# Kernel tuning notes

Measured on AMD Instinct MI355X. Metric: run time of the kernel, lower is better.

Reference implementation:

```python
import jax, jax.numpy as jnp
import numpy as np

E, T, D_IN, D_HID, D_OUT = 8, 2048, 1024, 4096, 1024
INTER = 2 * D_HID  # gated (SwiGLU) -> weight1 produces [gate, val]


def setup_inputs() -> dict:
    key = jax.random.key(0)
    k_x, k_w1, k_w2 = jax.random.split(key, 3)
    # kaiming_uniform-ish scale for weights
    x = jax.random.normal(k_x, (E, T, D_IN), dtype=jnp.float32)
    w1 = jax.random.normal(k_w1, (E, D_IN, INTER), dtype=jnp.float32) * (1.0 / np.sqrt(D_IN))
    w2 = jax.random.normal(k_w2, (E, D_HID, D_OUT), dtype=jnp.float32) * (1.0 / np.sqrt(D_HID))
    return {"x": x, "weight1": w1, "weight2": w2}


def reference(x, weight1, weight2):
    # h: [E, T, 2*D_HID] grouped GEMM over experts
    h = jnp.einsum("etd,edi->eti", x, weight1)
    gate, val = jnp.split(h, 2, axis=-1)
    h = jax.nn.silu(gate) * val  # SwiGLU; dropout is identity in eval / p=0
    out = jnp.einsum("eth,eho->eto", h, weight2)  # [E, T, D_OUT]
    return out
```

## Files before the change

### kernel.cpp

```cpp
#include <hip/hip_runtime.h>


#define E_    8
#define T_    2048
#define DIN   1024
#define DHID  4096
#define DOUT  1024
#define INTER 8192

typedef _Float16 f16;
typedef _Float16 f16x8 __attribute__((ext_vector_type(8)));
typedef float    f32x4 __attribute__((ext_vector_type(4)));

typedef const __attribute__((address_space(1))) void gvoid_t;
typedef __attribute__((address_space(3))) void lvoid_t;

__device__ __forceinline__ void gload_lds16(const void* g, void* l) {
  __builtin_amdgcn_global_load_lds((gvoid_t*)g, (lvoid_t*)l, 16, 0, 0);
}

__global__ __launch_bounds__(256) void conv_f32_f16(
    const float* __restrict__ src, f16* __restrict__ dst, int n8) {
  int i = blockIdx.x * 256 + threadIdx.x;
  int stride = gridDim.x * 256;
  for (; i < n8; i += stride) {
    const float4* s = (const float4*)(src + (size_t)i * 8);
    float4 a0 = s[0], a1 = s[1];
    f16x8 v;
    v[0] = (f16)a0.x; v[1] = (f16)a0.y; v[2] = (f16)a0.z; v[3] = (f16)a0.w;
    v[4] = (f16)a1.x; v[5] = (f16)a1.y; v[6] = (f16)a1.z; v[7] = (f16)a1.w;
    *(f16x8*)(dst + (size_t)i * 8) = v;
  }
}

__global__ __launch_bounds__(256) void xpose_f32_f16(
    const float* __restrict__ src, f16* __restrict__ dst,
    int R, int C, int tR, int tC) {
  __shared__ f16 tile[32][33];
  int bid = blockIdx.x;
  int perE = tR * tC;
  int e = bid / perE;
  int rem = bid - e * perE;
  int rt = rem / tC;
  int ct = rem - rt * tC;
  int r0 = rt * 32, c0 = ct * 32;
  int t = threadIdx.x;
  int lr = t >> 5, lc = t & 31;
  const float* s = src + (size_t)e * R * C;
  f16* d = dst + (size_t)e * C * R;
#pragma unroll
  for (int i = 0; i < 4; ++i) {
    int r = lr + 8 * i;
    tile[r][lc] = (f16)s[(size_t)(r0 + r) * C + (c0 + lc)];
  }
  __syncthreads();
#pragma unroll
  for (int i = 0; i < 4; ++i) {
    int r = lr + 8 * i;
    d[(size_t)(c0 + r) * R + (r0 + lc)] = tile[lc][r];
  }
}

__global__ __launch_bounds__(512, 2) void gemm1_swiglu_xh(
    const f16* __restrict__ xh,
    const f16* __restrict__ w1t,
    f16* __restrict__ hact) {
  __shared__ f16 As[128][32];
  __shared__ f16 Bg[128][32];
  __shared__ f16 Bv[128][32];

  int bid = blockIdx.x;
  int e   = bid >> 9;
  int rem = bid & 511;
  int mt  = rem >> 5;
  int nt  = rem & 31;
  int m0 = mt * 128, n0 = nt * 128;

  const f16* xe = xh  + ((size_t)e * T_ + m0) * DIN;
  const f16* wg = w1t + ((size_t)e * INTER + n0) * DIN;
  const f16* wv = w1t + ((size_t)e * INTER + DHID + n0) * DIN;

  int tid  = threadIdx.x;
  int lane = tid & 63;
  int wid  = tid >> 6;

  int srow = wid * 16 + (lane >> 2);
  int scol = (lane & 3) * 8;
  f16* lA = &As[wid * 16][0];
  f16* lG = &Bg[wid * 16][0];
  f16* lV = &Bv[wid * 16][0];

  int wm = wid >> 2;
  int wn = wid & 3;
  int lr = lane & 15;
  int lk = (lane >> 4) * 8;

  f32x4 accG[4][2], accV[4][2];
#pragma unroll
  for (int m = 0; m < 4; ++m)
#pragma unroll
    for (int n = 0; n < 2; ++n) {
      accG[m][n] = f32x4{0.f, 0.f, 0.f, 0.f};
      accV[m][n] = f32x4{0.f, 0.f, 0.f, 0.f};
    }

  for (int k = 0; k < DIN; k += 32) {
    __syncthreads();
    gload_lds16(xe + (size_t)srow * DIN + k + scol, lA);
    gload_lds16(wg + (size_t)srow * DIN + k + scol, lG);
    gload_lds16(wv + (size_t)srow * DIN + k + scol, lV);
    __syncthreads();

    f16x8 af[4], bg[2], bv[2];
#pragma unroll
    for (int m = 0; m < 4; ++m)
      af[m] = *(const f16x8*)&As[wm * 64 + m * 16 + lr][lk];
#pragma unroll
    for (int n = 0; n < 2; ++n) {
      bg[n] = *(const f16x8*)&Bg[wn * 32 + n * 16 + lr][lk];
      bv[n] = *(const f16x8*)&Bv[wn * 32 + n * 16 + lr][lk];
    }
#pragma unroll
    for (int m = 0; m < 4; ++m)
#pragma unroll
      for (int n = 0; n < 2; ++n) {
        accG[m][n] = __builtin_amdgcn_mfma_f32_16x16x32_f16(af[m], bg[n], accG[m][n], 0, 0, 0);
        accV[m][n] = __builtin_amdgcn_mfma_f32_16x16x32_f16(af[m], bv[n], accV[m][n], 0, 0, 0);
      }
  }

  f16* he = hact + (size_t)e * T_ * DHID;
  int rbase = m0 + wm * 64 + (lane >> 4) * 4;
  int cbase = n0 + wn * 32 + lr;
#pragma unroll
  for (int m = 0; m < 4; ++m)
#pragma unroll
    for (int n = 0; n < 2; ++n)
#pragma unroll
      for (int j = 0; j < 4; ++j) {
        int row = rbase + m * 16 + j;
        int col = cbase + n * 16;
        float g = accG[m][n][j];
        float v = accV[m][n][j];
        float s = g / (1.0f + __expf(-g));
        he[(size_t)row * DHID + col] = (f16)(s * v);
      }
}

__global__ __launch_bounds__(512, 2) void gemm1_swiglu_rs(
    const float* __restrict__ x,
    const f16* __restrict__ w1t,
    f16* __restrict__ hact) {
  __shared__ f16 As[128][36];
  __shared__ f16 Bg[128][32];
  __shared__ f16 Bv[128][32];

  int bid = blockIdx.x;
  int e   = bid >> 9;
  int rem = bid & 511;
  int mt  = rem >> 5;
  int nt  = rem & 31;
  int m0 = mt * 128, n0 = nt * 128;

  const float* xe = x   + ((size_t)e * T_ + m0) * DIN;
  const f16*   wg = w1t + ((size_t)e * INTER + n0) * DIN;
  const f16*   wv = w1t + ((size_t)e * INTER + DHID + n0) * DIN;

  int tid  = threadIdx.x;
  int lane = tid & 63;
  int wid  = tid >> 6;

  int arow = tid >> 2;
  int acol = (tid & 3) * 8;
  int brow = wid * 16 + (lane >> 2);
  int bcol = (lane & 3) * 8;
  f16* lG = &Bg[wid * 16][0];
  f16* lV = &Bv[wid * 16][0];

  int wm = wid >> 2;
  int wn = wid & 3;
  int lr = lane & 15;
  int lk = (lane >> 4) * 8;

  f32x4 accG[4][2], accV[4][2];
#pragma unroll
  for (int m = 0; m < 4; ++m)
#pragma unroll
    for (int n = 0; n < 2; ++n) {
      accG[m][n] = f32x4{0.f, 0.f, 0.f, 0.f};
      accV[m][n] = f32x4{0.f, 0.f, 0.f, 0.f};
    }

  for (int k = 0; k < DIN; k += 32) {
    __syncthreads();
    gload_lds16(wg + (size_t)brow * DIN + k + bcol, lG);
    gload_lds16(wv + (size_t)brow * DIN + k + bcol, lV);
    {
      const float* sa = xe + (size_t)arow * DIN + k + acol;
      float4 a0 = ((const float4*)sa)[0];
      float4 a1 = ((const float4*)sa)[1];
      f16x8 v;
      v[0] = (f16)a0.x; v[1] = (f16)a0.y; v[2] = (f16)a0.z; v[3] = (f16)a0.w;
      v[4] = (f16)a1.x; v[5] = (f16)a1.y; v[6] = (f16)a1.z; v[7] = (f16)a1.w;
      *(f16x8*)&As[arow][acol] = v;
    }
    __syncthreads();

    f16x8 af[4], bg[2], bv[2];
#pragma unroll
    for (int m = 0; m < 4; ++m)
      af[m] = *(const f16x8*)&As[wm * 64 + m * 16 + lr][lk];
#pragma unroll
    for (int n = 0; n < 2; ++n) {
      bg[n] = *(const f16x8*)&Bg[wn * 32 + n * 16 + lr][lk];
      bv[n] = *(const f16x8*)&Bv[wn * 32 + n * 16 + lr][lk];
    }
#pragma unroll
    for (int m = 0; m < 4; ++m)
#pragma unroll
      for (int n = 0; n < 2; ++n) {
        accG[m][n] = __builtin_amdgcn_mfma_f32_16x16x32_f16(af[m], bg[n], accG[m][n], 0, 0, 0);
        accV[m][n] = __builtin_amdgcn_mfma_f32_16x16x32_f16(af[m], bv[n], accV[m][n], 0, 0, 0);
      }
  }

  f16* he = hact + (size_t)e * T_ * DHID;
  int rbase = m0 + wm * 64 + (lane >> 4) * 4;
  int cbase = n0 + wn * 32 + lr;
#pragma unroll
  for (int m = 0; m < 4; ++m)
#pragma unroll
    for (int n = 0; n < 2; ++n)
#pragma unroll
      for (int j = 0; j < 4; ++j) {
        int row = rbase + m * 16 + j;
        int col = cbase + n * 16;
        float g = accG[m][n][j];
        float v = accV[m][n][j];
        float s = g / (1.0f + __expf(-g));
        he[(size_t)row * DHID + col] = (f16)(s * v);
      }
}

__global__ __launch_bounds__(256) void gemm2(
    const f16* __restrict__ hact,
    const f16* __restrict__ w2t,
    float* __restrict__ out) {
  __shared__ f16 As[128][32];
  __shared__ f16 Bs[128][32];

  int bid = blockIdx.x;
  int e   = bid >> 7;
  int rem = bid & 127;
  int mt  = rem >> 3;
  int nt  = rem & 7;
  int m0 = mt * 128, n0 = nt * 128;

  const f16* ha = hact + ((size_t)e * T_ + m0) * DHID;
  const f16* wb = w2t  + ((size_t)e * DOUT + n0) * DHID;

  int tid  = threadIdx.x;
  int lane = tid & 63;
  int wid  = tid >> 6;

  int srow0 = wid * 32 + (lane >> 2);
  int srow1 = srow0 + 16;
  int scol  = (lane & 3) * 8;
  f16* lA0 = &As[wid * 32][0];
  f16* lA1 = &As[wid * 32 + 16][0];
  f16* lB0 = &Bs[wid * 32][0];
  f16* lB1 = &Bs[wid * 32 + 16][0];

  int wm = wid >> 1;
  int wn = wid & 1;
  int lr = lane & 15;
  int lk = (lane >> 4) * 8;

  f32x4 acc[4][4];
#pragma unroll
  for (int m = 0; m < 4; ++m)
#pragma unroll
    for (int n = 0; n < 4; ++n) acc[m][n] = f32x4{0.f, 0.f, 0.f, 0.f};

  for (int k = 0; k < DHID; k += 32) {
    __syncthreads();
    gload_lds16(ha + (size_t)srow0 * DHID + k + scol, lA0);
    gload_lds16(ha + (size_t)srow1 * DHID + k + scol, lA1);
    gload_lds16(wb + (size_t)srow0 * DHID + k + scol, lB0);
    gload_lds16(wb + (size_t)srow1 * DHID + k + scol, lB1);
    __syncthreads();

    f16x8 af[4], bf[4];
#pragma unroll
    for (int m = 0; m < 4; ++m)
      af[m] = *(const f16x8*)&As[wm * 64 + m * 16 + lr][lk];
#pragma unroll
    for (int n = 0; n < 4; ++n)
      bf[n] = *(const f16x8*)&Bs[wn * 64 + n * 16 + lr][lk];
#pragma unroll
    for (int m = 0; m < 4; ++m)
#pragma unroll
      for (int n = 0; n < 4; ++n)
        acc[m][n] = __builtin_amdgcn_mfma_f32_16x16x32_f16(af[m], bf[n], acc[m][n], 0, 0, 0);
  }

  float* oe = out + (size_t)e * T_ * DOUT;
  int rbase = m0 + wm * 64 + (lane >> 4) * 4;
  int cbase = n0 + wn * 64 + lr;
#pragma unroll
  for (int m = 0; m < 4; ++m)
#pragma unroll
    for (int n = 0; n < 4; ++n)
#pragma unroll
      for (int j = 0; j < 4; ++j) {
        int row = rbase + m * 16 + j;
        int col = cbase + n * 16;
        oe[(size_t)row * DOUT + col] = acc[m][n][j];
      }
}

extern "C" void kernel_launch(void* const* d_in, const int* in_sizes, int n_in,
                              void* d_out, int out_size, void* d_ws, size_t ws_size,
                              hipStream_t stream) {
  const float* x  = (const float*)d_in[0];
  const float* w1 = (const float*)d_in[1];
  const float* w2 = (const float*)d_in[2];
  float* out = (float*)d_out;

  const size_t HACT_B = (size_t)E_ * T_ * DHID * 2;
  const size_t WT_B   = (size_t)E_ * INTER * DIN * 2;
  const size_t XH_B   = (size_t)E_ * T_ * DIN * 2;

  f16* hact = (f16*)d_ws;
  f16* wt   = (f16*)((char*)d_ws + HACT_B);

  xpose_f32_f16<<<E_ * (DIN / 32) * (INTER / 32), 256, 0, stream>>>(
      w1, wt, DIN, INTER, DIN / 32, INTER / 32);

  if (ws_size >= HACT_B + WT_B + XH_B) {
    f16* xxh = (f16*)((char*)d_ws + HACT_B + WT_B);
    conv_f32_f16<<<2048, 256, 0, stream>>>(x, xxh, E_ * T_ * DIN / 8);
    gemm1_swiglu_xh<<<E_ * 16 * 32, 512, 0, stream>>>(xxh, wt, hact);
  } else {
    gemm1_swiglu_rs<<<E_ * 16 * 32, 512, 0, stream>>>(x, wt, hact);
  }

  xpose_f32_f16<<<E_ * (DHID / 32) * (DOUT / 32), 256, 0, stream>>>(
      w2, wt, DHID, DOUT, DHID / 32, DOUT / 32);
  gemm2<<<E_ * 16 * 8, 256, 0, stream>>>(hact, wt, out);
}
```

Measured before the change: 685.5 us.

## Rewrite gemm1 SwiGLU kernel as 256x128 double-buffered eight-phase pipeline

Replaces the single-buffered 128x128, K=32 gemm1 kernel with a 256x128 tile using K=64 steps. LDS is double-buffered and XOR-swizzled, and global-to-LDS loads are interleaved across eight phases with MFMA bursts under raised wave priority. Block IDs are also remapped so consecutive blocks spread across experts. The aim is to hide global load latency, cut LDS bank conflicts and halve the number of A/B loads per output. In exchange it uses more registers (128 accumulators) and LDS, and relies on fragile hand-written vmcnt and barrier scheduling.

After: 682.2 us. About the same (-0.5%).

```diff
diff --git a/kernel.cpp b/kernel.cpp
--- a/kernel.cpp
+++ b/kernel.cpp
@@ -61,20 +61,21 @@
   }
 }
 
-__global__ __launch_bounds__(512, 2) void gemm1_swiglu_xh(
+__global__ __launch_bounds__(512, 2) void gemm1_swiglu_8ph(
     const f16* __restrict__ xh,
     const f16* __restrict__ w1t,
     f16* __restrict__ hact) {
-  __shared__ f16 As[128][32];
-  __shared__ f16 Bg[128][32];
-  __shared__ f16 Bv[128][32];
-
-  int bid = blockIdx.x;
-  int e   = bid >> 9;
-  int rem = bid & 511;
+  __shared__ __align__(1024) f16 As [2][256][64];
+  __shared__ __align__(1024) f16 Bgs[2][128][64];
+  __shared__ __align__(1024) f16 Bvs[2][128][64];
+
+  int bid0 = blockIdx.x;
+  int bid  = (bid0 & 7) * 256 + (bid0 >> 3);
+  int e   = bid >> 8;
+  int rem = bid & 255;
   int mt  = rem >> 5;
   int nt  = rem & 31;
-  int m0 = mt * 128, n0 = nt * 128;
+  int m0 = mt * 256, n0 = nt * 128;
 
   const f16* xe = xh  + ((size_t)e * T_ + m0) * DIN;
   const f16* wg = w1t + ((size_t)e * INTER + n0) * DIN;
@@ -83,57 +84,144 @@
   int tid  = threadIdx.x;
   int lane = tid & 63;
   int wid  = tid >> 6;
-
-  int srow = wid * 16 + (lane >> 2);
-  int scol = (lane & 3) * 8;
-  f16* lA = &As[wid * 16][0];
-  f16* lG = &Bg[wid * 16][0];
-  f16* lV = &Bv[wid * 16][0];
-
-  int wm = wid >> 2;
-  int wn = wid & 3;
-  int lr = lane & 15;
-  int lk = (lane >> 4) * 8;
-
-  f32x4 accG[4][2], accV[4][2];
-#pragma unroll
-  for (int m = 0; m < 4; ++m)
+  int wm   = wid >> 2;
+  int wn   = wid & 3;
+  int lr   = lane & 15;
+  int l16  = lane >> 4;
+
+  int srow = lane >> 3;
+  int scol = ((lane & 7) ^ srow) * 8;
+
+  auto stageA = [&](int buf, int kt, int i) {
+    int ci = wid + 8 * i;
+    gload_lds16(xe + (size_t)(ci * 8 + srow) * DIN + kt * 64 + scol,
+                (char*)&As[buf][0][0] + ci * 1024);
+  };
+  auto stageG = [&](int buf, int kt, int i) {
+    int ci = wid + 8 * i;
+    gload_lds16(wg + (size_t)(ci * 8 + srow) * DIN + kt * 64 + scol,
+                (char*)&Bgs[buf][0][0] + ci * 1024);
+  };
+  auto stageV = [&](int buf, int kt, int i) {
+    int ci = wid + 8 * i;
+    gload_lds16(wv + (size_t)(ci * 8 + srow) * DIN + kt * 64 + scol,
+                (char*)&Bvs[buf][0][0] + ci * 1024);
+  };
+
+  f32x4 accG[8][2], accV[8][2];
+#pragma unroll
+  for (int m = 0; m < 8; ++m)
 #pragma unroll
     for (int n = 0; n < 2; ++n) {
       accG[m][n] = f32x4{0.f, 0.f, 0.f, 0.f};
       accV[m][n] = f32x4{0.f, 0.f, 0.f, 0.f};
     }
 
-  for (int k = 0; k < DIN; k += 32) {
-    __syncthreads();
-    gload_lds16(xe + (size_t)srow * DIN + k + scol, lA);
-    gload_lds16(wg + (size_t)srow * DIN + k + scol, lG);
-    gload_lds16(wv + (size_t)srow * DIN + k + scol, lV);
-    __syncthreads();
-
-    f16x8 af[4], bg[2], bv[2];
-#pragma unroll
-    for (int m = 0; m < 4; ++m)
-      af[m] = *(const f16x8*)&As[wm * 64 + m * 16 + lr][lk];
-#pragma unroll
-    for (int n = 0; n < 2; ++n) {
-      bg[n] = *(const f16x8*)&Bg[wn * 32 + n * 16 + lr][lk];
-      bv[n] = *(const f16x8*)&Bv[wn * 32 + n * 16 + lr][lk];
-    }
-#pragma unroll
-    for (int m = 0; m < 4; ++m)
-#pragma unroll
-      for (int n = 0; n < 2; ++n) {
-        accG[m][n] = __builtin_amdgcn_mfma_f32_16x16x32_f16(af[m], bg[n], accG[m][n], 0, 0, 0);
-        accV[m][n] = __builtin_amdgcn_mfma_f32_16x16x32_f16(af[m], bv[n], accV[m][n], 0, 0, 0);
-      }
-  }
+  f16x8 af[4][2], bg[2][2], bv[2][2];
+
+#define READ_AF(b, MH)                                                       \
+  _Pragma("unroll") for (int m = 0; m < 4; ++m)                              \
+  _Pragma("unroll") for (int kk = 0; kk < 2; ++kk) {                         \
+    int row_ = wm * 128 + (MH) * 64 + m * 16 + lr;                           \
+    af[m][kk] = *(const f16x8*)((const char*)&As[b][0][0] + row_ * 128 +     \
+                                (((kk * 4 + l16) ^ (lr & 7)) << 4));         \
+  }
+#define READ_B(ARR, DST, b)                                                  \
+  _Pragma("unroll") for (int n = 0; n < 2; ++n)                              \
+  _Pragma("unroll") for (int kk = 0; kk < 2; ++kk) {                         \
+    int row_ = wn * 32 + n * 16 + lr;                                        \
+    DST[n][kk] = *(const f16x8*)((const char*)&ARR[b][0][0] + row_ * 128 +   \
+                                 (((kk * 4 + l16) ^ (lr & 7)) << 4));        \
+  }
+#define MFMA16(ACC, BB, MH)                                                  \
+  __builtin_amdgcn_s_setprio(1);                                            \
+  _Pragma("unroll") for (int m = 0; m < 4; ++m)                              \
+  _Pragma("unroll") for (int n = 0; n < 2; ++n)                              \
+  _Pragma("unroll") for (int kk = 0; kk < 2; ++kk)                          \
+    ACC[(MH) * 4 + m][n] = __builtin_amdgcn_mfma_f32_16x16x32_f16(           \
+        af[m][kk], BB[n][kk], ACC[(MH) * 4 + m][n], 0, 0, 0);                \
+  __builtin_amdgcn_s_setprio(0);
+#define BAR() __builtin_amdgcn_s_barrier()
+#define LGKM0() asm volatile("s_waitcnt lgkmcnt(0)" ::: "memory")
+#define VM6() asm volatile("s_waitcnt vmcnt(6)" ::: "memory")
+
+  stageA(0, 0, 0); stageA(0, 0, 1); stageA(0, 0, 2); stageA(0, 0, 3);
+  stageG(0, 0, 0); stageG(0, 0, 1);
+  stageV(0, 0, 0); stageV(0, 0, 1);
+  stageA(1, 1, 0); stageA(1, 1, 1);
+  stageG(1, 1, 0); stageG(1, 1, 1);
+  stageV(1, 1, 0); stageV(1, 1, 1);
+  VM6();
+  BAR();
+
+  for (int it = 0; it < 8; ++it) {
+    int tb = 2 * it + 1;
+    int pa = (2 * it + 2) & 15;
+    int pb = (2 * it + 3) & 15;
+
+    READ_AF(0, 0);
+    READ_B(Bgs, bg, 0);
+    stageA(1, tb, 2); stageA(1, tb, 3);
+    BAR(); LGKM0();
+    MFMA16(accG, bg, 0);
+    BAR();
+
+    READ_B(Bvs, bv, 0);
+    stageG(0, pa, 0); stageG(0, pa, 1);
+    BAR(); LGKM0();
+    MFMA16(accV, bv, 0);
+    BAR();
+
+    READ_AF(0, 1);
+    stageV(0, pa, 0); stageV(0, pa, 1);
+    BAR(); LGKM0();
+    MFMA16(accG, bg, 1);
+    BAR();
+
+    stageA(0, pa, 0); stageA(0, pa, 1);
+    BAR();
+    MFMA16(accV, bv, 1);
+    VM6();
+    BAR();
+
+    READ_AF(1, 0);
+    READ_B(Bgs, bg, 1);
+    stageA(0, pa, 2); stageA(0, pa, 3);
+    BAR(); LGKM0();
+    MFMA16(accG, bg, 0);
+    BAR();
+
+    READ_B(Bvs, bv, 1);
+    stageG(1, pb, 0); stageG(1, pb, 1);
+    BAR(); LGKM0();
+    MFMA16(accV, bv, 0);
+    BAR();
+
+    READ_AF(1, 1);
+    stageV(1, pb, 0); stageV(1, pb, 1);
+    BAR(); LGKM0();
+    MFMA16(accG, bg, 1);
+    BAR();
+
+    stageA(1, pb, 0); stageA(1, pb, 1);
+    BAR();
+    MFMA16(accV, bv, 1);
+    VM6();
+    BAR();
+  }
+
+#undef READ_AF
+#undef READ_B
+#undef MFMA16
+#undef BAR
+#undef LGKM0
+#undef VM6
 
   f16* he = hact + (size_t)e * T_ * DHID;
-  int rbase = m0 + wm * 64 + (lane >> 4) * 4;
+  int rbase = m0 + wm * 128 + l16 * 4;
   int cbase = n0 + wn * 32 + lr;
 #pragma unroll
-  for (int m = 0; m < 4; ++m)
+  for (int m = 0; m < 8; ++m)
 #pragma unroll
     for (int n = 0; n < 2; ++n)
 #pragma unroll
@@ -340,7 +428,7 @@
   if (ws_size >= HACT_B + WT_B + XH_B) {
     f16* xxh = (f16*)((char*)d_ws + HACT_B + WT_B);
     conv_f32_f16<<<2048, 256, 0, stream>>>(x, xxh, E_ * T_ * DIN / 8);
-    gemm1_swiglu_xh<<<E_ * 16 * 32, 512, 0, stream>>>(xxh, wt, hact);
+    gemm1_swiglu_8ph<<<E_ * 8 * 32, 512, 0, stream>>>(xxh, wt, hact);
   } else {
     gemm1_swiglu_rs<<<E_ * 16 * 32, 512, 0, stream>>>(x, wt, hact);
   }
```

## Rewrite gemm2 as 256x256 double-buffered 8-phase pipelined MFMA kernel

Applied to the files above, without the earlier changes.

Replaces the simple single-buffered 128x128 GEMM2 with a 256x256-tile, 512-thread kernel. It uses K=64 double-buffered LDS tiles with XOR swizzling and issues global-to-LDS loads interleaved across eight barrier-separated phases. MFMA priority is raised during the math phases. The aim is to overlap memory traffic with compute, raise reuse per loaded byte, and avoid LDS bank conflicts, at the cost of higher register and LDS use and fewer blocks.

Result: faster. 600.4 us (-12.4%).

```diff
diff --git a/kernel.cpp b/kernel.cpp
--- a/kernel.cpp
+++ b/kernel.cpp
@@ -242,19 +242,19 @@
       }
 }
 
-__global__ __launch_bounds__(256) void gemm2(
+__global__ __launch_bounds__(512, 2) void gemm2_8ph(
     const f16* __restrict__ hact,
     const f16* __restrict__ w2t,
     float* __restrict__ out) {
-  __shared__ f16 As[128][32];
-  __shared__ f16 Bs[128][32];
+  __shared__ __align__(1024) f16 As[2][256][64];
+  __shared__ __align__(1024) f16 Bs[2][256][64];
 
   int bid = blockIdx.x;
-  int e   = bid >> 7;
-  int rem = bid & 127;
-  int mt  = rem >> 3;
-  int nt  = rem & 7;
-  int m0 = mt * 128, n0 = nt * 128;
+  int e   = bid >> 5;
+  int rem = bid & 31;
+  int mt  = rem >> 2;
+  int nt  = rem & 3;
+  int m0 = mt * 256, n0 = nt * 256;
 
   const f16* ha = hact + ((size_t)e * T_ + m0) * DHID;
   const f16* wb = w2t  + ((size_t)e * DOUT + n0) * DHID;
@@ -262,53 +262,132 @@
   int tid  = threadIdx.x;
   int lane = tid & 63;
   int wid  = tid >> 6;
-
-  int srow0 = wid * 32 + (lane >> 2);
-  int srow1 = srow0 + 16;
-  int scol  = (lane & 3) * 8;
-  f16* lA0 = &As[wid * 32][0];
-  f16* lA1 = &As[wid * 32 + 16][0];
-  f16* lB0 = &Bs[wid * 32][0];
-  f16* lB1 = &Bs[wid * 32 + 16][0];
-
-  int wm = wid >> 1;
-  int wn = wid & 1;
-  int lr = lane & 15;
-  int lk = (lane >> 4) * 8;
-
-  f32x4 acc[4][4];
-#pragma unroll
-  for (int m = 0; m < 4; ++m)
+  int wm   = wid >> 2;
+  int wn   = wid & 3;
+  int lr   = lane & 15;
+  int l16  = lane >> 4;
+
+  int srow = lane >> 3;
+  int scol = ((lane & 7) ^ srow) * 8;
+
+  auto stA = [&](int buf, int kt, int i) {
+    int ci = wid + 8 * i;
+    gload_lds16(ha + (size_t)(ci * 8 + srow) * DHID + kt * 64 + scol,
+                (char*)&As[buf][0][0] + ci * 1024);
+  };
+  auto stB = [&](int buf, int kt, int i) {
+    int ci = wid + 8 * i;
+    gload_lds16(wb + (size_t)(ci * 8 + srow) * DHID + kt * 64 + scol,
+                (char*)&Bs[buf][0][0] + ci * 1024);
+  };
+
+  f32x4 acc[8][4];
+#pragma unroll
+  for (int m = 0; m < 8; ++m)
 #pragma unroll
     for (int n = 0; n < 4; ++n) acc[m][n] = f32x4{0.f, 0.f, 0.f, 0.f};
 
-  for (int k = 0; k < DHID; k += 32) {
-    __syncthreads();
-    gload_lds16(ha + (size_t)srow0 * DHID + k + scol, lA0);
-    gload_lds16(ha + (size_t)srow1 * DHID + k + scol, lA1);
-    gload_lds16(wb + (size_t)srow0 * DHID + k + scol, lB0);
-    gload_lds16(wb + (size_t)srow1 * DHID + k + scol, lB1);
-    __syncthreads();
-
-    f16x8 af[4], bf[4];
-#pragma unroll
-    for (int m = 0; m < 4; ++m)
-      af[m] = *(const f16x8*)&As[wm * 64 + m * 16 + lr][lk];
-#pragma unroll
-    for (int n = 0; n < 4; ++n)
-      bf[n] = *(const f16x8*)&Bs[wn * 64 + n * 16 + lr][lk];
-#pragma unroll
-    for (int m = 0; m < 4; ++m)
-#pragma unroll
-      for (int n = 0; n < 4; ++n)
-        acc[m][n] = __builtin_amdgcn_mfma_f32_16x16x32_f16(af[m], bf[n], acc[m][n], 0, 0, 0);
-  }
+  f16x8 af[4][2], bf0[2][2], bf1[2][2];
+
+#define READ_A2(b, MH)                                                       \
+  _Pragma("unroll") for (int m = 0; m < 4; ++m)                              \
+  _Pragma("unroll") for (int kk = 0; kk < 2; ++kk) {                         \
+    int row_ = wm * 128 + (MH) * 64 + m * 16 + lr;                           \
+    af[m][kk] = *(const f16x8*)((const char*)&As[b][0][0] + row_ * 128 +     \
+                                (((kk * 4 + l16) ^ (lr & 7)) << 4));         \
+  }
+#define READ_B2(b, NH, DST)                                                  \
+  _Pragma("unroll") for (int n = 0; n < 2; ++n)                              \
+  _Pragma("unroll") for (int kk = 0; kk < 2; ++kk) {                         \
+    int row_ = wn * 64 + (NH) * 32 + n * 16 + lr;                            \
+    DST[n][kk] = *(const f16x8*)((const char*)&Bs[b][0][0] + row_ * 128 +    \
+                                 (((kk * 4 + l16) ^ (lr & 7)) << 4));        \
+  }
+#define MFMA16Q(MH, NH, BB)                                                  \
+  __builtin_amdgcn_s_setprio(1);                                            \
+  _Pragma("unroll") for (int m = 0; m < 4; ++m)                              \
+  _Pragma("unroll") for (int n = 0; n < 2; ++n)                              \
+  _Pragma("unroll") for (int kk = 0; kk < 2; ++kk)                          \
+    acc[(MH) * 4 + m][(NH) * 2 + n] = __builtin_amdgcn_mfma_f32_16x16x32_f16(\
+        af[m][kk], BB[n][kk], acc[(MH) * 4 + m][(NH) * 2 + n], 0, 0, 0);     \
+  __builtin_amdgcn_s_setprio(0);
+#define BAR() __builtin_amdgcn_s_barrier()
+#define LGKM0() asm volatile("s_waitcnt lgkmcnt(0)" ::: "memory")
+#define VM6() asm volatile("s_waitcnt vmcnt(6)" ::: "memory")
+
+  stA(0, 0, 0); stA(0, 0, 1); stA(0, 0, 2); stA(0, 0, 3);
+  stB(0, 0, 0); stB(0, 0, 1); stB(0, 0, 2); stB(0, 0, 3);
+  stB(1, 1, 0); stB(1, 1, 1); stB(1, 1, 2); stB(1, 1, 3);
+  stA(1, 1, 0); stA(1, 1, 1);
+  VM6();
+  BAR();
+
+  for (int it = 0; it < 32; ++it) {
+    int tb = 2 * it + 1;
+    int pa = (2 * it + 2) & 63;
+    int pb = (2 * it + 3) & 63;
+
+    READ_A2(0, 0); READ_B2(0, 0, bf0);
+    stA(1, tb, 2); stA(1, tb, 3);
+    BAR(); LGKM0();
+    MFMA16Q(0, 0, bf0);
+    BAR();
+
+    READ_B2(0, 1, bf1);
+    BAR(); LGKM0();
+    MFMA16Q(0, 1, bf1);
+    BAR();
+
+    READ_A2(0, 1);
+    stB(0, pa, 0); stB(0, pa, 1);
+    BAR(); LGKM0();
+    MFMA16Q(1, 0, bf0);
+    BAR();
+
+    stB(0, pa, 2); stB(0, pa, 3);
+    stA(0, pa, 0); stA(0, pa, 1);
+    BAR();
+    MFMA16Q(1, 1, bf1);
+    VM6();
+    BAR();
+
+    READ_A2(1, 0); READ_B2(1, 0, bf0);
+    stA(0, pa, 2); stA(0, pa, 3);
+    BAR(); LGKM0();
+    MFMA16Q(0, 0, bf0);
+    BAR();
+
+    READ_B2(1, 1, bf1);
+    BAR(); LGKM0();
+    MFMA16Q(0, 1, bf1);
+    BAR();
+
+    READ_A2(1, 1);
+    stB(1, pb, 0); stB(1, pb, 1);
+    BAR(); LGKM0();
+    MFMA16Q(1, 0, bf0);
+    BAR();
+
+    stB(1, pb, 2); stB(1, pb, 3);
+    stA(1, pb, 0); stA(1, pb, 1);
+    BAR();
+    MFMA16Q(1, 1, bf1);
+    VM6();
+    BAR();
+  }
+
+#undef READ_A2
+#undef READ_B2
+#undef MFMA16Q
+#undef BAR
+#undef LGKM0
+#undef VM6
 
   float* oe = out + (size_t)e * T_ * DOUT;
-  int rbase = m0 + wm * 64 + (lane >> 4) * 4;
+  int rbase = m0 + wm * 128 + l16 * 4;
   int cbase = n0 + wn * 64 + lr;
 #pragma unroll
-  for (int m = 0; m < 4; ++m)
+  for (int m = 0; m < 8; ++m)
 #pragma unroll
     for (int n = 0; n < 4; ++n)
 #pragma unroll
@@ -347,5 +426,5 @@
 
   xpose_f32_f16<<<E_ * (DHID / 32) * (DOUT / 32), 256, 0, stream>>>(
       w2, wt, DHID, DOUT, DHID / 32, DOUT / 32);
-  gemm2<<<E_ * 16 * 8, 256, 0, stream>>>(hact, wt, out);
-}
+  gemm2_8ph<<<E_ * 8 * 4, 512, 0, stream>>>(hact, wt, out);
+}
```
